# Kernel optimization log

Hardware: AMD Instinct MI355X
Metric: run time of the kernel (lower is better)

The kernel has to match this reference:

```python
import jax, jax.numpy as jnp
import numpy as np

EMBED_DIM = 768
NUM_HEADS = 12
HEAD_DIM = EMBED_DIM // NUM_HEADS


def setup_inputs() -> dict:
    key = jax.random.key(0)
    k_x, k_wqkv, k_bqkv, k_wp, k_bp = jax.random.split(key, 5)
    B, N, C = 4, 2048, EMBED_DIM
    # torch nn.Linear init scale ~ 1/sqrt(fan_in); use small normal for numerics
    s = 1.0 / np.sqrt(C)
    return {
        "x": jax.random.normal(k_x, (B, N, C), dtype=jnp.float32),
        "w_qkv": jax.random.normal(k_wqkv, (3 * C, C), dtype=jnp.float32) * s,  # torch [out,in]
        "b_qkv": jax.random.normal(k_bqkv, (3 * C,), dtype=jnp.float32) * s,
        "w_proj": jax.random.normal(k_wp, (C, C), dtype=jnp.float32) * s,
        "b_proj": jax.random.normal(k_bp, (C,), dtype=jnp.float32) * s,
    }


def reference(x, w_qkv, b_qkv, w_proj, b_proj):
    B, N, C = x.shape
    H, D = NUM_HEADS, HEAD_DIM
    scale = 1.0 / np.sqrt(D)
    # qkv linear: x @ W.T + b  -> [B,N,3C]
    qkv = jnp.einsum("bnc,oc->bno", x, w_qkv) + b_qkv
    qkv = qkv.reshape(B, N, 3, H, D).transpose(2, 0, 3, 1, 4)  # [3,B,H,N,D]
    q, k, v = qkv[0], qkv[1], qkv[2]
    attn = jnp.einsum("bhnd,bhmd->bhnm", q, k) * scale  # [B,H,N,N]
    attn = jax.nn.softmax(attn, axis=-1)
    out = jnp.einsum("bhnm,bhmd->bhnd", attn, v)  # [B,H,N,D]
    out = out.transpose(0, 2, 1, 3).reshape(B, N, C)
    return jnp.einsum("bnc,oc->bno", out, w_proj) + b_proj
```

## Files before the change

### kernel.cpp

```cpp
#include <hip/hip_runtime.h>
#include <hip/hip_bf16.h>
#include <math.h>

#define EMBED 768
#define NHEAD 12
#define HDIM 64
#define SEQ 2048
#define BATCH 4

typedef __hip_bfloat16 bf16;
typedef __attribute__((ext_vector_type(8))) short bf16x8;
typedef __attribute__((ext_vector_type(4))) short s16x4;
typedef __attribute__((ext_vector_type(4))) float f32x4;
typedef __attribute__((ext_vector_type(2))) unsigned int u32x2;

__device__ inline float b2f(bf16 v) { return __bfloat162float(v); }
__device__ inline bf16 f2b(float v) { return __float2bfloat16(v); }
__device__ inline unsigned pk2(float a, float b) {
  return (unsigned)__bfloat16_as_ushort(f2b(a)) |
         ((unsigned)__bfloat16_as_ushort(f2b(b)) << 16);
}

__device__ inline void gl_lds16(const bf16* g, bf16* l) {
  __builtin_amdgcn_global_load_lds(
      (const __attribute__((address_space(1))) void*)g,
      (__attribute__((address_space(3))) void*)l, 16, 0, 0);
}

#define NX4  (BATCH * SEQ * EMBED / 4)
#define NWQ4 (3 * EMBED * EMBED / 4)
#define NWP4 (EMBED * EMBED / 4)

__global__ __launch_bounds__(256) void cvt_all(
    const float* __restrict__ x, const float* __restrict__ wq,
    const float* __restrict__ wp, bf16* __restrict__ xb,
    bf16* __restrict__ wqb, bf16* __restrict__ wpb) {
  int i = blockIdx.x * 256 + threadIdx.x;
  const float* src;
  bf16* dst;
  int k;
  if (i < NX4) {
    src = x; dst = xb; k = i;
  } else if (i < NX4 + NWQ4) {
    src = wq; dst = wqb; k = i - NX4;
  } else if (i < NX4 + NWQ4 + NWP4) {
    src = wp; dst = wpb; k = i - NX4 - NWQ4;
  } else {
    return;
  }
  float4 v = ((const float4*)src)[k];
  s16x4 o;
  o[0] = (short)__bfloat16_as_ushort(f2b(v.x));
  o[1] = (short)__bfloat16_as_ushort(f2b(v.y));
  o[2] = (short)__bfloat16_as_ushort(f2b(v.z));
  o[3] = (short)__bfloat16_as_ushort(f2b(v.w));
  *(s16x4*)(dst + 4 * (size_t)k) = o;
}

__global__ __launch_bounds__(512, 2) void gemm_qkv(
    const bf16* __restrict__ A, const bf16* __restrict__ W,
    const float* __restrict__ bias, bf16* __restrict__ outQ,
    bf16* __restrict__ outK, bf16* __restrict__ outV, int K) {
  __shared__ bf16 As[2][256][64];
  __shared__ bf16 Bs[2][256][64];
  const int t = threadIdx.x;
  const int w = t >> 6;
  const int lane = t & 63;
  const int g = lane >> 4, c = lane & 15;
  const int m0 = blockIdx.y * 256, n0 = blockIdx.x * 256;
  const int wr = (w >> 2) * 128;
  const int wc = (w & 3) * 64;

  const int srow = lane >> 3;
  const int l8 = lane & 7;
  const int sseg = (l8 ^ srow) * 8;

  f32x4 acc[4][8] = {};
  const int nsteps = K >> 6;

#pragma unroll
  for (int i = 0; i < 4; i++) {
    int r = w * 32 + i * 8;
    gl_lds16(A + (size_t)(m0 + r + srow) * K + sseg, &As[0][r][0]);
    gl_lds16(W + (size_t)(n0 + r + srow) * K + sseg, &Bs[0][r][0]);
  }
  __syncthreads();

  for (int s = 0; s < nsteps; s++) {
    const int p = s & 1;
    if (s + 1 < nsteps) {
      const int k0 = (s + 1) << 6;
#pragma unroll
      for (int i = 0; i < 4; i++) {
        int r = w * 32 + i * 8;
        gl_lds16(A + (size_t)(m0 + r + srow) * K + k0 + sseg, &As[p ^ 1][r][0]);
        gl_lds16(W + (size_t)(n0 + r + srow) * K + k0 + sseg, &Bs[p ^ 1][r][0]);
      }
    }

#pragma unroll
    for (int h = 0; h < 2; h++) {
      bf16x8 xf[8], wf[4];
#pragma unroll
      for (int j = 0; j < 8; j++)
        xf[j] = *(const bf16x8*)&As[p][wr + j * 16 + c][((h * 4 + g) ^ (c & 7)) * 8];
#pragma unroll
      for (int i = 0; i < 4; i++)
        wf[i] = *(const bf16x8*)&Bs[p][wc + i * 16 + c][((h * 4 + g) ^ (c & 7)) * 8];
#pragma unroll
      for (int i = 0; i < 4; i++)
#pragma unroll
        for (int j = 0; j < 8; j++)
          acc[i][j] = __builtin_amdgcn_mfma_f32_16x16x32_bf16(wf[i], xf[j],
                                                              acc[i][j], 0, 0, 0);
    }
    __syncthreads();
  }

#pragma unroll
  for (int i = 0; i < 4; i++) {
    const int ob = n0 + wc + i * 16 + g * 4;
    const f32x4 bv = *(const f32x4*)&bias[ob];
    const int which = ob / EMBED;
    const int rem = ob - which * EMBED;
    const int hh = rem >> 6;
    const int d0 = rem & 63;
#pragma unroll
    for (int j = 0; j < 8; j++) {
      const int m = m0 + wr + j * 16 + c;
      f32x4 v = acc[i][j] + bv;
      const int bb = m >> 11, n = m & 2047;
      const size_t bh = (size_t)bb * NHEAD + hh;
      if (which == 0) {
        s16x4 q4;
#pragma unroll
        for (int r = 0; r < 4; r++)
          q4[r] = (short)__bfloat16_as_ushort(f2b(v[r] * 0.1803368801f));
        *(s16x4*)&outQ[(bh * SEQ + n) * HDIM + d0] = q4;
      } else if (which == 1) {
        s16x4 k4;
#pragma unroll
        for (int r = 0; r < 4; r++)
          k4[r] = (short)__bfloat16_as_ushort(f2b(v[r]));
        *(s16x4*)&outK[(bh * SEQ + n) * HDIM + d0] = k4;
      } else {
#pragma unroll
        for (int r = 0; r < 4; r++)
          outV[(bh * HDIM + d0 + r) * SEQ + n] = f2b(v[r]);
      }
    }
  }
}

template <int TM>
__global__ __launch_bounds__(256, 4) void gemm_proj(
    const bf16* __restrict__ A, const bf16* __restrict__ W,
    const float* __restrict__ bias, float* __restrict__ outF, int N, int K) {
  __shared__ bf16 As[TM][64];
  __shared__ bf16 Bs[128][64];
  const int t = threadIdx.x;
  const int w = t >> 6;
  const int lane = t & 63;
  const int g = lane >> 4, c = lane & 15;
  const int m0 = blockIdx.y * TM, n0 = blockIdx.x * 128;
  constexpr int MJ = TM / 32;
  const int wr = (w >> 1) * (TM / 2);
  const int wc = (w & 1) * 64;

  const int srow = lane >> 3;
  const int l8 = lane & 7;
  const int sseg = (l8 ^ srow) * 8;

  f32x4 acc[4][MJ] = {};

  for (int k0 = 0; k0 < K; k0 += 64) {
#pragma unroll
    for (int i = 0; i < 4; i++) {
      int r = w * 32 + i * 8;
      gl_lds16(W + (size_t)(n0 + r + srow) * K + k0 + sseg, &Bs[r][0]);
    }
#pragma unroll
    for (int i = 0; i < TM / 32; i++) {
      int r = w * (TM / 4) + i * 8;
      gl_lds16(A + (size_t)(m0 + r + srow) * K + k0 + sseg, &As[r][0]);
    }
    __syncthreads();

#pragma unroll
    for (int h = 0; h < 2; h++) {
      bf16x8 xf[MJ], wf[4];
#pragma unroll
      for (int j = 0; j < MJ; j++)
        xf[j] = *(const bf16x8*)&As[wr + j * 16 + c][((h * 4 + g) ^ (c & 7)) * 8];
#pragma unroll
      for (int i = 0; i < 4; i++)
        wf[i] = *(const bf16x8*)&Bs[wc + i * 16 + c][((h * 4 + g) ^ (c & 7)) * 8];
#pragma unroll
      for (int i = 0; i < 4; i++)
#pragma unroll
        for (int j = 0; j < MJ; j++)
          acc[i][j] = __builtin_amdgcn_mfma_f32_16x16x32_bf16(wf[i], xf[j],
                                                              acc[i][j], 0, 0, 0);
    }
    __syncthreads();
  }

#pragma unroll
  for (int i = 0; i < 4; i++) {
    const int ob = n0 + wc + i * 16 + g * 4;
    const f32x4 bv = *(const f32x4*)&bias[ob];
#pragma unroll
    for (int j = 0; j < MJ; j++) {
      const int m = m0 + wr + j * 16 + c;
      f32x4 v = acc[i][j] + bv;
      *(f32x4*)&outF[(size_t)m * N + ob] = v;
    }
  }
}

__global__ __launch_bounds__(256, 4) void attn_mfma(
    const bf16* __restrict__ Q, const bf16* __restrict__ Kk,
    const bf16* __restrict__ V, bf16* __restrict__ O) {
  __shared__ bf16 Ks[64 * 64];
  __shared__ bf16 Vts[64 * 64];
  __shared__ bf16 Pt[8][16 * 72];

  const int blk = blockIdx.x;
  const int bh = blk >> 4;
  const int qt = blk & 15;
  const int bb = bh / NHEAD;
  const int h = bh % NHEAD;
  const int t = threadIdx.x;
  const int lane = t & 63;
  const int w = t >> 6;
  const int g = lane >> 4;
  const int c = lane & 15;
  const size_t base = (size_t)bh * SEQ * HDIM;
  const int mb0 = qt * 128 + w * 16;
  const int mb1 = mb0 + 64;

  const int r8 = lane >> 3;
  const int l8 = lane & 7;
  const int gch = l8 ^ (r8 & 7);
  const int q0 = w * 2, q1 = w * 2 + 1;

  bf16x8 qa[2][2];
#pragma unroll
  for (int kh = 0; kh < 2; kh++) {
    qa[0][kh] = *(const bf16x8*)(Q + base + (size_t)(mb0 + c) * HDIM + kh * 32 + g * 8);
    qa[1][kh] = *(const bf16x8*)(Q + base + (size_t)(mb1 + c) * HDIM + kh * 32 + g * 8);
  }

  bf16x8 ones;
#pragma unroll
  for (int i = 0; i < 8; i++) ones[i] = (short)0x3F80;

  f32x4 o[2][4] = {};
  f32x4 o_l[2] = {};

  gl_lds16(Kk + base + (size_t)(q0 * 8 + r8) * HDIM + gch * 8, &Ks[q0 * 8 * 64]);
  gl_lds16(Kk + base + (size_t)(q1 * 8 + r8) * HDIM + gch * 8, &Ks[q1 * 8 * 64]);
  gl_lds16(V + base + (size_t)(q0 * 8 + r8) * SEQ + gch * 8, &Vts[q0 * 8 * 64]);
  gl_lds16(V + base + (size_t)(q1 * 8 + r8) * SEQ + gch * 8, &Vts[q1 * 8 * 64]);
  __syncthreads();

  bf16* const Pt0 = Pt[w * 2];
  bf16* const Pt1 = Pt[w * 2 + 1];

  for (int jt = 0; jt < SEQ / 64; jt++) {
    f32x4 s[2][4] = {};
#pragma unroll
    for (int nt = 0; nt < 4; nt++) {
#pragma unroll
      for (int kh = 0; kh < 2; kh++) {
        bf16x8 kb = *(const bf16x8*)&Ks[(nt * 16 + c) * 64 + ((kh * 4 + g) ^ (c & 7)) * 8];
        s[0][nt] = __builtin_amdgcn_mfma_f32_16x16x32_bf16(kb, qa[0][kh], s[0][nt], 0, 0, 0);
        s[1][nt] = __builtin_amdgcn_mfma_f32_16x16x32_bf16(kb, qa[1][kh], s[1][nt], 0, 0, 0);
      }
    }

    __syncthreads();
    if (jt + 1 < SEQ / 64) {
      const int jb = (jt + 1) * 64;
      gl_lds16(Kk + base + (size_t)(jb + q0 * 8 + r8) * HDIM + gch * 8, &Ks[q0 * 8 * 64]);
      gl_lds16(Kk + base + (size_t)(jb + q1 * 8 + r8) * HDIM + gch * 8, &Ks[q1 * 8 * 64]);
    }

#pragma unroll
    for (int nt = 0; nt < 4; nt++) {
      float a0 = __builtin_amdgcn_exp2f(s[0][nt][0]);
      float a1 = __builtin_amdgcn_exp2f(s[0][nt][1]);
      float a2 = __builtin_amdgcn_exp2f(s[0][nt][2]);
      float a3 = __builtin_amdgcn_exp2f(s[0][nt][3]);
      u32x2 pw0 = {pk2(a0, a1), pk2(a2, a3)};
      *(u32x2*)&Pt0[c * 72 + nt * 16 + g * 4] = pw0;
      float b0 = __builtin_amdgcn_exp2f(s[1][nt][0]);
      float b1 = __builtin_amdgcn_exp2f(s[1][nt][1]);
      float b2 = __builtin_amdgcn_exp2f(s[1][nt][2]);
      float b3 = __builtin_amdgcn_exp2f(s[1][nt][3]);
      u32x2 pw1 = {pk2(b0, b1), pk2(b2, b3)};
      *(u32x2*)&Pt1[c * 72 + nt * 16 + g * 4] = pw1;
    }
    bf16x8 pb[2][2];
    pb[0][0] = *(const bf16x8*)&Pt0[c * 72 + g * 8];
    pb[0][1] = *(const bf16x8*)&Pt0[c * 72 + 32 + g * 8];
    pb[1][0] = *(const bf16x8*)&Pt1[c * 72 + g * 8];
    pb[1][1] = *(const bf16x8*)&Pt1[c * 72 + 32 + g * 8];

#pragma unroll
    for (int dt = 0; dt < 4; dt++) {
      bf16x8 vb0 = *(const bf16x8*)&Vts[(dt * 16 + c) * 64 + ((0 + g) ^ (c & 7)) * 8];
      bf16x8 vb1 = *(const bf16x8*)&Vts[(dt * 16 + c) * 64 + ((4 + g) ^ (c & 7)) * 8];
      o[0][dt] = __builtin_amdgcn_mfma_f32_16x16x32_bf16(vb0, pb[0][0], o[0][dt], 0, 0, 0);
      o[0][dt] = __builtin_amdgcn_mfma_f32_16x16x32_bf16(vb1, pb[0][1], o[0][dt], 0, 0, 0);
      o[1][dt] = __builtin_amdgcn_mfma_f32_16x16x32_bf16(vb0, pb[1][0], o[1][dt], 0, 0, 0);
      o[1][dt] = __builtin_amdgcn_mfma_f32_16x16x32_bf16(vb1, pb[1][1], o[1][dt], 0, 0, 0);
    }
    o_l[0] = __builtin_amdgcn_mfma_f32_16x16x32_bf16(ones, pb[0][0], o_l[0], 0, 0, 0);
    o_l[0] = __builtin_amdgcn_mfma_f32_16x16x32_bf16(ones, pb[0][1], o_l[0], 0, 0, 0);
    o_l[1] = __builtin_amdgcn_mfma_f32_16x16x32_bf16(ones, pb[1][0], o_l[1], 0, 0, 0);
    o_l[1] = __builtin_amdgcn_mfma_f32_16x16x32_bf16(ones, pb[1][1], o_l[1], 0, 0, 0);

    __syncthreads();
    if (jt + 1 < SEQ / 64) {
      const int jb = (jt + 1) * 64;
      gl_lds16(V + base + (size_t)(q0 * 8 + r8) * SEQ + jb + gch * 8, &Vts[q0 * 8 * 64]);
      gl_lds16(V + base + (size_t)(q1 * 8 + r8) * SEQ + jb + gch * 8, &Vts[q1 * 8 * 64]);
    }
  }

#pragma unroll
  for (int grp = 0; grp < 2; grp++) {
    const float inv = __builtin_amdgcn_rcpf(o_l[grp][0]);
    const int mb = grp ? mb1 : mb0;
    const size_t rowoff = ((size_t)bb * SEQ + mb + c) * EMBED + h * 64 + g * 4;
#pragma unroll
    for (int dt = 0; dt < 4; dt++) {
      s16x4 ov;
#pragma unroll
      for (int r = 0; r < 4; r++)
        ov[r] = (short)__bfloat16_as_ushort(f2b(o[grp][dt][r] * inv));
      *(s16x4*)&O[rowoff + dt * 16] = ov;
    }
  }
}

extern "C" void kernel_launch(void* const* d_in, const int* in_sizes, int n_in,
                              void* d_out, int out_size, void* d_ws,
                              size_t ws_size, hipStream_t stream) {
  const float* x      = (const float*)d_in[0];
  const float* w_qkv  = (const float*)d_in[1];
  const float* b_qkv  = (const float*)d_in[2];
  const float* w_proj = (const float*)d_in[3];
  const float* b_proj = (const float*)d_in[4];

  const size_t per = (size_t)BATCH * NHEAD * SEQ * HDIM;
  bf16* Qp = (bf16*)d_ws;
  bf16* Kp = Qp + per;
  bf16* Vp = Kp + per;
  bf16* xb = Vp + per;
  bf16* wqkvb = xb + per;
  bf16* wprojb = wqkvb + (size_t)3 * EMBED * EMBED;
  bf16* AO = xb;

  const int ncvt = NX4 + NWQ4 + NWP4;
  cvt_all<<<dim3((ncvt + 255) / 256), 256, 0, stream>>>(x, w_qkv, w_proj, xb,
                                                        wqkvb, wprojb);

  dim3 g1(2304 / 256, 8192 / 256);
  gemm_qkv<<<g1, 512, 0, stream>>>(xb, wqkvb, b_qkv, Qp, Kp, Vp, EMBED);

  attn_mfma<<<dim3(BATCH * NHEAD * (SEQ / 128)), 256, 0, stream>>>(Qp, Kp, Vp, AO);

  dim3 g2(768 / 128, 8192 / 64);
  gemm_proj<64><<<g2, 256, 0, stream>>>(AO, wprojb, b_proj, (float*)d_out,
                                        EMBED, EMBED);
}
```

Before: 233.3 us.

## Restructure QKV GEMM pipeline with staggered prefetch and XCD-aware block mapping

Rewrites the QKV GEMM main loop into four sub-phases per k-step. Each sub-phase issues part of the next tile's global-to-LDS loads, uses explicit vmcnt waits and raw barriers, and raises wave priority around the MFMA bursts. The W tile is prefetched two steps ahead into the current buffer, and W fragments are held in registers across the sub-phases. Both GEMMs switch to a 1D grid remapped so consecutive blocks on the same XCD share A rows, aiming for better L2 reuse. The projection GEMM's occupancy hint is raised to 5. This adds more barriers per step and makes correctness depend on the hand-written waitcnt ordering.

```diff
diff --git a/kernel.cpp b/kernel.cpp
--- a/kernel.cpp
+++ b/kernel.cpp
@@ -60,61 +60,104 @@
 __global__ __launch_bounds__(512, 2) void gemm_qkv(
     const bf16* __restrict__ A, const bf16* __restrict__ W,
     const float* __restrict__ bias, bf16* __restrict__ outQ,
-    bf16* __restrict__ outK, bf16* __restrict__ outV, int K) {
+    bf16* __restrict__ outK, bf16* __restrict__ outV) {
   __shared__ bf16 As[2][256][64];
   __shared__ bf16 Bs[2][256][64];
+  constexpr int KK = EMBED;
+  constexpr int NSTEP = KK / 64;
+
   const int t = threadIdx.x;
   const int w = t >> 6;
   const int lane = t & 63;
   const int g = lane >> 4, c = lane & 15;
-  const int m0 = blockIdx.y * 256, n0 = blockIdx.x * 256;
+
+  const int bid = blockIdx.x;
+  const int xcd = bid & 7, idx = bid >> 3;
+  const int m0 = (xcd * 4 + idx / 9) * 256;
+  const int n0 = (idx % 9) * 256;
+
   const int wr = (w >> 2) * 128;
   const int wc = (w & 3) * 64;
 
-  const int srow = lane >> 3;
-  const int l8 = lane & 7;
-  const int sseg = (l8 ^ srow) * 8;
+  const int r8 = lane >> 3;
+  const int sseg = ((lane & 7) ^ r8) * 8;
+
+  auto stage = [&](const bf16* mat, int row0, int kt, bf16* dst) {
+#pragma unroll
+    for (int rnd = 0; rnd < 2; rnd++) {
+      const int rb = (rnd * 8 + w) * 8;
+      gl_lds16(mat + (size_t)(row0 + rb + r8) * KK + kt * 64 + sseg,
+               dst + rb * 64);
+    }
+  };
 
   f32x4 acc[4][8] = {};
-  const int nsteps = K >> 6;
-
-#pragma unroll
-  for (int i = 0; i < 4; i++) {
-    int r = w * 32 + i * 8;
-    gl_lds16(A + (size_t)(m0 + r + srow) * K + sseg, &As[0][r][0]);
-    gl_lds16(W + (size_t)(n0 + r + srow) * K + sseg, &Bs[0][r][0]);
-  }
-  __syncthreads();
-
-  for (int s = 0; s < nsteps; s++) {
+  bf16x8 wf[4][2];
+
+  stage(A, m0, 0, &As[0][0][0]);
+  stage(A, m0 + 128, 0, &As[0][128][0]);
+  stage(W, n0, 0, &Bs[0][0][0]);
+  stage(W, n0 + 128, 0, &Bs[0][128][0]);
+  stage(W, n0, 1, &Bs[1][0][0]);
+  stage(W, n0 + 128, 1, &Bs[1][128][0]);
+  asm volatile("s_waitcnt vmcnt(4)" ::: "memory");
+  __builtin_amdgcn_s_barrier();
+  asm volatile("" ::: "memory");
+
+  for (int s = 0; s < NSTEP; s++) {
     const int p = s & 1;
-    if (s + 1 < nsteps) {
-      const int k0 = (s + 1) << 6;
-#pragma unroll
-      for (int i = 0; i < 4; i++) {
-        int r = w * 32 + i * 8;
-        gl_lds16(A + (size_t)(m0 + r + srow) * K + k0 + sseg, &As[p ^ 1][r][0]);
-        gl_lds16(W + (size_t)(n0 + r + srow) * K + k0 + sseg, &Bs[p ^ 1][r][0]);
+#pragma unroll
+    for (int q = 0; q < 4; q++) {
+      bf16x8 xf[2][2];
+#pragma unroll
+      for (int d = 0; d < 2; d++)
+#pragma unroll
+        for (int kh = 0; kh < 2; kh++)
+          xf[d][kh] = *(const bf16x8*)
+              &As[p][wr + (q * 2 + d) * 16 + c][((kh * 4 + g) ^ (c & 7)) * 8];
+      if (q == 0) {
+#pragma unroll
+        for (int i = 0; i < 4; i++)
+#pragma unroll
+          for (int kh = 0; kh < 2; kh++)
+            wf[i][kh] = *(const bf16x8*)
+                &Bs[p][wc + i * 16 + c][((kh * 4 + g) ^ (c & 7)) * 8];
       }
-    }
-
-#pragma unroll
-    for (int h = 0; h < 2; h++) {
-      bf16x8 xf[8], wf[4];
-#pragma unroll
-      for (int j = 0; j < 8; j++)
-        xf[j] = *(const bf16x8*)&As[p][wr + j * 16 + c][((h * 4 + g) ^ (c & 7)) * 8];
+
+      if (q == 0) {
+        if (s + 1 < NSTEP) stage(A, m0, s + 1, &As[p ^ 1][0][0]);
+      } else if (q == 1) {
+        if (s + 1 < NSTEP) stage(A, m0 + 128, s + 1, &As[p ^ 1][128][0]);
+      } else if (q == 2) {
+        if (s + 2 < NSTEP) stage(W, n0, s + 2, &Bs[p][0][0]);
+      } else {
+        if (s + 2 < NSTEP) {
+          stage(W, n0 + 128, s + 2, &Bs[p][128][0]);
+          asm volatile("s_waitcnt vmcnt(4)" ::: "memory");
+        } else {
+          asm volatile("s_waitcnt vmcnt(0)" ::: "memory");
+        }
+      }
+
+      asm volatile("" ::: "memory");
+      __builtin_amdgcn_s_barrier();
+      asm volatile("" ::: "memory");
+
+      __builtin_amdgcn_s_setprio(1);
 #pragma unroll
       for (int i = 0; i < 4; i++)
-        wf[i] = *(const bf16x8*)&Bs[p][wc + i * 16 + c][((h * 4 + g) ^ (c & 7)) * 8];
-#pragma unroll
-      for (int i = 0; i < 4; i++)
-#pragma unroll
-        for (int j = 0; j < 8; j++)
-          acc[i][j] = __builtin_amdgcn_mfma_f32_16x16x32_bf16(wf[i], xf[j],
-                                                              acc[i][j], 0, 0, 0);
-    }
-    __syncthreads();
+#pragma unroll
+        for (int d = 0; d < 2; d++)
+#pragma unroll
+          for (int kh = 0; kh < 2; kh++)
+            acc[i][q * 2 + d] = __builtin_amdgcn_mfma_f32_16x16x32_bf16(
+                wf[i][kh], xf[d][kh], acc[i][q * 2 + d], 0, 0, 0);
+      __builtin_amdgcn_s_setprio(0);
+
+      asm volatile("" ::: "memory");
+      __builtin_amdgcn_s_barrier();
+      asm volatile("" ::: "memory");
+    }
   }
 
 #pragma unroll
@@ -152,17 +195,24 @@
   }
 }
 
-template <int TM>
-__global__ __launch_bounds__(256, 4) void gemm_proj(
+__global__ __launch_bounds__(256, 5) void gemm_proj(
     const bf16* __restrict__ A, const bf16* __restrict__ W,
     const float* __restrict__ bias, float* __restrict__ outF, int N, int K) {
+  constexpr int TM = 64;
   __shared__ bf16 As[TM][64];
   __shared__ bf16 Bs[128][64];
   const int t = threadIdx.x;
   const int w = t >> 6;
   const int lane = t & 63;
   const int g = lane >> 4, c = lane & 15;
-  const int m0 = blockIdx.y * TM, n0 = blockIdx.x * 128;
+
+  const int bid = blockIdx.x;
+  const int xcd = bid & 7;
+  const int idx = bid >> 3;
+  const int mr = xcd * 16 + idx / 6;
+  const int nc = idx % 6;
+  const int m0 = mr * TM, n0 = nc * 128;
+
   constexpr int MJ = TM / 32;
   const int wr = (w >> 1) * (TM / 2);
   const int wc = (w & 1) * 64;
@@ -367,12 +417,10 @@
   cvt_all<<<dim3((ncvt + 255) / 256), 256, 0, stream>>>(x, w_qkv, w_proj, xb,
                                                         wqkvb, wprojb);
 
-  dim3 g1(2304 / 256, 8192 / 256);
-  gemm_qkv<<<g1, 512, 0, stream>>>(xb, wqkvb, b_qkv, Qp, Kp, Vp, EMBED);
+  gemm_qkv<<<dim3(288), 512, 0, stream>>>(xb, wqkvb, b_qkv, Qp, Kp, Vp);
 
   attn_mfma<<<dim3(BATCH * NHEAD * (SEQ / 128)), 256, 0, stream>>>(Qp, Kp, Vp, AO);
 
-  dim3 g2(768 / 128, 8192 / 64);
-  gemm_proj<64><<<g2, 256, 0, stream>>>(AO, wprojb, b_proj, (float*)d_out,
-                                        EMBED, EMBED);
-}
+  gemm_proj<<<dim3(768), 256, 0, stream>>>(AO, wprojb, b_proj, (float*)d_out,
+                                           EMBED, EMBED);
+}
```

Result: slower. 238.5 us (+2.2%).
